# Kernel tuning notes

Measured on AMD Instinct MI355X. Metric: run time of the kernel, lower is better.

## Reference

```python
import jax, jax.numpy as jnp
import numpy as np

STRIDES = (8, 16, 32)
BINS = 16
NC = 80
ALPHA, GAMMA = 0.25, 2.0
W_CLS, W_IOU, W_DFL = 1.0, 7.5, 1.5
B, MAX_GT = 32, 32
EPS = 1e-7


def setup_inputs() -> dict:
    key = jax.random.key(0)
    k0, k1, k2, k3, k4, k5, k6 = jax.random.split(key, 7)
    p0 = jax.random.normal(k0, (B, 4 * BINS + NC, 80, 80), dtype=jnp.float32)
    p1 = jax.random.normal(k1, (B, 4 * BINS + NC, 40, 40), dtype=jnp.float32)
    p2 = jax.random.normal(k2, (B, 4 * BINS + NC, 20, 20), dtype=jnp.float32)
    # realistic xyxy boxes inside a 640x640 image
    c = jax.random.uniform(k3, (B, MAX_GT, 2), minval=60.0, maxval=580.0)
    wh = jax.random.uniform(k4, (B, MAX_GT, 2), minval=16.0, maxval=120.0)
    gt_bboxes = jnp.concatenate([c - wh / 2, c + wh / 2], axis=-1).astype(jnp.float32)
    gt_labels = jax.random.randint(k5, (B, MAX_GT), 0, NC, dtype=jnp.int32)
    raw = jax.random.randint(k6, (B, 8400), 0, 20 * MAX_GT, dtype=jnp.int32)
    matched_gt_inds = jnp.where(raw < MAX_GT, raw, -1)
    return {"p0": p0, "p1": p1, "p2": p2, "gt_bboxes": gt_bboxes,
            "gt_labels": gt_labels, "matched_gt_inds": matched_gt_inds}


def _decode_scale(p, stride):
    # p: [B, 4*BINS + NC, H, W]
    Bp, C, H, W = p.shape
    dfl = p[:, :4 * BINS].reshape(Bp, 4, BINS, H, W)
    cls = p[:, 4 * BINS:]
    # DFL decode: expectation of softmax over bins, scaled by stride
    prob = jax.nn.softmax(dfl, axis=2)
    proj = jnp.arange(BINS, dtype=p.dtype)
    dist = jnp.einsum('bkchw,c->bkhw', prob, proj) * stride  # [B,4,H,W] in pixels
    ys, xs = jnp.meshgrid(jnp.arange(H), jnp.arange(W), indexing='ij')
    cx = ((xs.astype(p.dtype)) + 0.5) * stride
    cy = ((ys.astype(p.dtype)) + 0.5) * stride
    boxes = jnp.stack([cx - dist[:, 0], cy - dist[:, 1],
                       cx + dist[:, 2], cy + dist[:, 3]], axis=-1).reshape(Bp, H * W, 4)
    cls_logits = cls.transpose(0, 2, 3, 1).reshape(Bp, H * W, NC)
    dfl_flat = dfl.transpose(0, 3, 4, 1, 2).reshape(Bp, H * W, 4, BINS)
    grid = jnp.stack([cx, cy], axis=-1).reshape(H * W, 2)
    smap = jnp.full((H * W,), stride, dtype=p.dtype)
    return cls_logits, dfl_flat, boxes, grid, smap


def reference(p0, p1, p2, gt_bboxes, gt_labels, matched_gt_inds):
    outs = [_decode_scale(p, s) for p, s in zip((p0, p1, p2), STRIDES)]
    scores = jnp.concatenate([o[0] for o in outs], axis=1)   # [B,N,NC]
    dfl = jnp.concatenate([o[1] for o in outs], axis=1)      # [B,N,4,BINS]
    pboxes = jnp.concatenate([o[2] for o in outs], axis=1)   # [B,N,4]
    grid = jnp.concatenate([o[3] for o in outs], axis=0)     # [N,2]
    smap = jnp.concatenate([o[4] for o in outs], axis=0)     # [N]

    pos = matched_gt_inds >= 0                               # [B,N]
    idx = jnp.where(pos, matched_gt_inds, 0)
    lbl = jnp.take_along_axis(gt_labels, idx, axis=1)        # [B,N]
    posf = pos.astype(scores.dtype)
    tgt_scores = jax.nn.one_hot(lbl, NC, dtype=scores.dtype) * posf[..., None]

    # sigmoid focal loss (stable BCE-with-logits)
    prob = jax.nn.sigmoid(scores)
    ce = jnp.maximum(scores, 0) - scores * tgt_scores + jnp.log1p(jnp.exp(-jnp.abs(scores)))
    p_t = prob * tgt_scores + (1 - prob) * (1 - tgt_scores)
    alpha_t = tgt_scores * ALPHA + (1 - tgt_scores) * (1 - ALPHA)
    cls_elem = alpha_t * (1.0 - p_t) ** GAMMA * ce
    num_pos = jnp.maximum(posf.sum(), 1.0)
    loss_cls = cls_elem.sum() / num_pos

    # gather matched GT boxes per anchor
    tboxes = jnp.take_along_axis(gt_bboxes, idx[..., None], axis=1)  # [B,N,4]
    gx, gy = grid[None, :, 0], grid[None, :, 1]
    l = jnp.clip(gx - tboxes[..., 0], 0.0)
    t = jnp.clip(gy - tboxes[..., 1], 0.0)
    r = jnp.clip(tboxes[..., 2] - gx, 0.0)
    b_ = jnp.clip(tboxes[..., 3] - gy, 0.0)
    dists = jnp.stack([l, t, r, b_], axis=-1) / smap[None, :, None]   # [B,N,4]
    tb = jnp.clip(dists, 0.0, BINS - 1 - 1e-6)
    lo = jnp.floor(tb).astype(jnp.int32)
    hi = jnp.minimum(lo + 1, BINS - 1)
    a = tb - lo.astype(tb.dtype)
    # soft two-bin DFL target (vectorized form of the scatter_add loop)
    tdist = (jax.nn.one_hot(lo, BINS, dtype=dfl.dtype) * (1.0 - a)[..., None]
             + jax.nn.one_hot(hi, BINS, dtype=dfl.dtype) * a[..., None])   # [B,N,4,BINS]
    logp = jax.nn.log_softmax(dfl, axis=-1)
    dfl_elem = -(tdist * logp).sum(-1)                                # [B,N,4]
    loss_dfl = (dfl_elem * posf[..., None]).sum() / (num_pos * 4.0)

    # IoU loss on positives
    ix1 = jnp.maximum(pboxes[..., 0], tboxes[..., 0])
    iy1 = jnp.maximum(pboxes[..., 1], tboxes[..., 1])
    ix2 = jnp.minimum(pboxes[..., 2], tboxes[..., 2])
    iy2 = jnp.minimum(pboxes[..., 3], tboxes[..., 3])
    inter = jnp.clip(ix2 - ix1, 0.0) * jnp.clip(iy2 - iy1, 0.0)
    area_p = jnp.clip(pboxes[..., 2] - pboxes[..., 0], 0.0) * jnp.clip(pboxes[..., 3] - pboxes[..., 1], 0.0)
    area_t = jnp.clip(tboxes[..., 2] - tboxes[..., 0], 0.0) * jnp.clip(tboxes[..., 3] - tboxes[..., 1], 0.0)
    iou = inter / (area_p + area_t - inter + EPS)
    loss_iou = ((1.0 - iou) * posf).sum() / num_pos

    total = W_CLS * loss_cls + W_IOU * loss_iou + W_DFL * loss_dfl
    return total
```

## Files before the change

kernel.cpp:

```cpp
#include <hip/hip_runtime.h>
#include <math.h>

#define NCLS 80
#define BINS 16
#define BATCH 32
#define MAX_GT 32
#define NA 8400
#define AN (BATCH * NA)
#define NT 2100
#define NQG (BATCH * NT)
#define NB_DFL 263
#define NB_CLS 5120
#define NSLOT 64
#define ALPHA_C 0.25f
#define W_CLS 1.0
#define W_IOU 7.5
#define W_DFL 1.5
#define EPS_F 1e-7f


__device__ __forceinline__ void block_reduce_atomic_16(float val, double* __restrict__ target)
{
    __shared__ float s[16];
    __syncthreads();
    #pragma unroll
    for (int o = 32; o > 0; o >>= 1) val += __shfl_down(val, o);
    const int wave = threadIdx.x >> 6, lane = threadIdx.x & 63;
    if (lane == 0) s[wave] = val;
    __syncthreads();
    if (threadIdx.x == 0) {
        float t = 0.f;
        #pragma unroll
        for (int i = 0; i < 16; ++i) t += s[i];
        atomicAdd(target, (double)t);
    }
}

__device__ __forceinline__ void block_reduce_atomic_4(float val, double* __restrict__ target)
{
    __shared__ float s[4];
    __syncthreads();
    #pragma unroll
    for (int o = 32; o > 0; o >>= 1) val += __shfl_down(val, o);
    const int wave = threadIdx.x >> 6, lane = threadIdx.x & 63;
    if (lane == 0) s[wave] = val;
    __syncthreads();
    if (threadIdx.x == 0) atomicAdd(target, (double)(s[0] + s[1] + s[2] + s[3]));
}

__device__ __forceinline__ float focal_elem(float s, float tt)
{
    float e   = __expf(-fabsf(s));
    float inv = 1.f / (1.f + e);
    float prob = (s >= 0.f) ? inv : e * inv;
    float ce  = fmaxf(s, 0.f) - s * tt + __logf(1.f + e);
    float p_t = prob * tt + (1.f - prob) * (1.f - tt);
    float alpha_t = tt * ALPHA_C + (1.f - tt) * (1.f - ALPHA_C);
    float om = 1.f - p_t;
    return alpha_t * om * om * ce;
}

__device__ __forceinline__ void quad_map(int t, int& HW, int& off, int& gbase,
                                         int& h, int& w0, float& stride)
{
    if (t < 1600)      { HW = 6400; off = t * 4;          gbase = 0;    stride = 8.f;
                         h = t / 20;  w0 = (t - h * 20) * 4; }
    else if (t < 2000) { HW = 1600; off = (t - 1600) * 4; gbase = 6400; stride = 16.f;
                         int u = t - 1600; h = u / 10; w0 = (u - h * 10) * 4; }
    else               { HW = 400;  off = (t - 2000) * 4; gbase = 8000; stride = 32.f;
                         int u = t - 2000; h = u / 5;  w0 = (u - h * 5) * 4; }
}

__global__ __launch_bounds__(256) void yolo_prep(
    const int* __restrict__ matched, const int* __restrict__ gt_labels,
    signed char* __restrict__ lblmap, double* __restrict__ acc)
{
    if (blockIdx.x == 0) acc[threadIdx.x] = 0.0;
    const int qid = blockIdx.x * 256 + threadIdx.x;
    if (qid >= AN / 4) return;
    const int a0 = qid * 4;
    const int b  = a0 / NA;
    const int4 m4 = *(const int4*)(matched + a0);
    const int mm[4] = {m4.x, m4.y, m4.z, m4.w};
    char4 o;
    o.x = (mm[0] >= 0) ? (signed char)gt_labels[b * MAX_GT + mm[0]] : (signed char)-1;
    o.y = (mm[1] >= 0) ? (signed char)gt_labels[b * MAX_GT + mm[1]] : (signed char)-1;
    o.z = (mm[2] >= 0) ? (signed char)gt_labels[b * MAX_GT + mm[2]] : (signed char)-1;
    o.w = (mm[3] >= 0) ? (signed char)gt_labels[b * MAX_GT + mm[3]] : (signed char)-1;
    *(char4*)(lblmap + a0) = o;
}

__global__ __launch_bounds__(1024, 8) void yolo_mega(
    const float* __restrict__ p0, const float* __restrict__ p1, const float* __restrict__ p2,
    const float* __restrict__ gt_bboxes, const int* __restrict__ matched,
    const signed char* __restrict__ lblmap, double* __restrict__ acc)
{
    const int bid  = blockIdx.x;
    const int slot = bid & (NSLOT - 1);

    if (bid < NB_DFL) {
        __shared__ float4 spd[4][256];
        const int local = threadIdx.x & 255;
        const int k     = threadIdx.x >> 8;
        const int qg    = bid * 256 + local;
        const bool valid = (qg < NQG);
        const int qv = valid ? qg : 0;
        const int b  = qv / NT;
        const int t  = qv - b * NT;

        int HW, off, gbase, h, w0; float stride;
        quad_map(t, HW, off, gbase, h, w0, stride);
        const float inv_s = 1.f / stride;
        const float cy = ((float)h + 0.5f) * stride;
        const float* p = (t < 1600) ? p0 : (t < 2000) ? p1 : p2;

        const int4 m4 = *(const int4*)(matched + (size_t)b * NA + gbase + off);
        const int mm[4] = {m4.x, m4.y, m4.z, m4.w};
        int lo[4]; float fr[4]; bool pos[4];
        #pragma unroll
        for (int j = 0; j < 4; ++j) {
            pos[j] = (mm[j] >= 0);
            int idx = pos[j] ? mm[j] : 0;
            float4 tb = *(const float4*)(gt_bboxes + ((size_t)b * MAX_GT + idx) * 4);
            float cx = ((float)(w0 + j) + 0.5f) * stride;
            float d = (k == 0) ? (cx - tb.x) : (k == 1) ? (cy - tb.y)
                    : (k == 2) ? (tb.z - cx) : (tb.w - cy);
            float tval = fminf(fmaxf(d, 0.f) * inv_s, (float)(BINS - 1) - 1e-6f);
            lo[j] = (int)floorf(tval);
            fr[j] = tval - (float)lo[j];
        }

        const float* pc = p + (size_t)(b * 144 + k * BINS) * HW + off;
        float mx[4], se[4], we[4], vlo[4], vhi[4];
        #pragma unroll
        for (int j = 0; j < 4; ++j) { mx[j] = -1e30f; se[j] = 0.f; we[j] = 0.f; vlo[j] = 0.f; vhi[j] = 0.f; }

        #pragma unroll 4
        for (int i = 0; i < BINS; ++i) {
            float4 q = {0.f, 0.f, 0.f, 0.f};
            if (valid) q = *(const float4*)(pc + (size_t)i * HW);
            const float vj[4] = {q.x, q.y, q.z, q.w};
            #pragma unroll
            for (int j = 0; j < 4; ++j) {
                float v = vj[j];
                float nm = fmaxf(mx[j], v);
                float scale = __expf(mx[j] - nm);
                float e = __expf(v - nm);
                se[j] = se[j] * scale + e;
                we[j] = we[j] * scale + (float)i * e;
                mx[j] = nm;
                vlo[j] = (i == lo[j])     ? v : vlo[j];
                vhi[j] = (i == lo[j] + 1) ? v : vhi[j];
            }
        }

        float part = 0.f;
        float pd[4];
        #pragma unroll
        for (int j = 0; j < 4; ++j) {
            pd[j] = (we[j] / se[j]) * stride;
            if (valid && pos[j]) {
                float lse = mx[j] + __logf(se[j]);
                part += -((1.f - fr[j]) * (vlo[j] - lse) + fr[j] * (vhi[j] - lse));
            }
        }
        spd[k][local] = make_float4(pd[0], pd[1], pd[2], pd[3]);
        __syncthreads();

        float iou_part = 0.f, cnt = 0.f;
        if (k == 0 && valid) {
            const float4 q0 = spd[0][local], q1 = spd[1][local];
            const float4 q2 = spd[2][local], q3 = spd[3][local];
            const float l_[4] = {q0.x, q0.y, q0.z, q0.w};
            const float t_[4] = {q1.x, q1.y, q1.z, q1.w};
            const float r_[4] = {q2.x, q2.y, q2.z, q2.w};
            const float b_[4] = {q3.x, q3.y, q3.z, q3.w};
            #pragma unroll
            for (int j = 0; j < 4; ++j) {
                if (pos[j]) {
                    float4 tb = *(const float4*)(gt_bboxes + ((size_t)b * MAX_GT + mm[j]) * 4);
                    float cx = ((float)(w0 + j) + 0.5f) * stride;
                    float px1 = cx - l_[j], py1 = cy - t_[j];
                    float px2 = cx + r_[j], py2 = cy + b_[j];
                    float ix1 = fmaxf(px1, tb.x), iy1 = fmaxf(py1, tb.y);
                    float ix2 = fminf(px2, tb.z), iy2 = fminf(py2, tb.w);
                    float inter  = fmaxf(ix2 - ix1, 0.f) * fmaxf(iy2 - iy1, 0.f);
                    float area_p = fmaxf(px2 - px1, 0.f) * fmaxf(py2 - py1, 0.f);
                    float area_t = fmaxf(tb.z - tb.x, 0.f) * fmaxf(tb.w - tb.y, 0.f);
                    float iou = inter / (area_p + area_t - inter + EPS_F);
                    iou_part += 1.f - iou;
                    cnt += 1.f;
                }
            }
        }
        block_reduce_atomic_16(part,     &acc[2 * NSLOT + slot]);
        block_reduce_atomic_16(iou_part, &acc[1 * NSLOT + slot]);
        block_reduce_atomic_16(cnt,      &acc[3 * NSLOT + slot]);
    } else {
        const int cbid  = bid - NB_DFL;
        const int half  = cbid & 1;
        const int plane = cbid >> 1;
        const int b = plane / NCLS;
        const int c = plane - b * NCLS;
        const size_t cls_ch = (size_t)(b * 144 + 4 * BINS + c);
        const signed char* lb0 = lblmap + b * NA;

        float part = 0.f;
        for (int q = (int)threadIdx.x; q < 1050; q += 1024) {
            const int t = half * 1050 + q;
            const float* p; int HW, off, gbase;
            if (t < 1600)      { p = p0; HW = 6400; off = t * 4;          gbase = 0;    }
            else if (t < 2000) { p = p1; HW = 1600; off = (t - 1600) * 4; gbase = 6400; }
            else               { p = p2; HW = 400;  off = (t - 2000) * 4; gbase = 8000; }

            float4 s4 = *(const float4*)(p + cls_ch * HW + off);
            char4  l4 = *(const char4*)(lb0 + gbase + off);
            part += focal_elem(s4.x, (c == l4.x) ? 1.f : 0.f);
            part += focal_elem(s4.y, (c == l4.y) ? 1.f : 0.f);
            part += focal_elem(s4.z, (c == l4.z) ? 1.f : 0.f);
            part += focal_elem(s4.w, (c == l4.w) ? 1.f : 0.f);
        }
        block_reduce_atomic_16(part, &acc[0 * NSLOT + slot]);
    }
}

__global__ __launch_bounds__(256) void yolo_loss_fused(
    const float* __restrict__ p0, const float* __restrict__ p1, const float* __restrict__ p2,
    const float* __restrict__ gt_bboxes, const int* __restrict__ gt_labels,
    const int* __restrict__ matched, double* __restrict__ acc)
{
    const int a = blockIdx.x * blockDim.x + threadIdx.x;
    const int b = blockIdx.y;
    const int slot = blockIdx.x & (NSLOT - 1);
    float cls_acc = 0.f, iou_acc = 0.f, dfl_acc = 0.f, pos_cnt = 0.f;
    if (a < NA) {
        const float* p; int HW, W; float stride; int off;
        if (a < 6400)      { p = p0; HW = 6400; W = 80; stride = 8.f;  off = a; }
        else if (a < 8000) { p = p1; HW = 1600; W = 40; stride = 16.f; off = a - 6400; }
        else               { p = p2; HW = 400;  W = 20; stride = 32.f; off = a - 8000; }
        const int h = off / W, w = off - h * W;
        const float cx = ((float)w + 0.5f) * stride, cy = ((float)h + 0.5f) * stride;
        const float* pb = p + ((size_t)b * 144) * (size_t)HW + (size_t)off;
        const int m = matched[(size_t)b * NA + a];
        const bool pos = (m >= 0);
        const int idx = pos ? m : 0;
        const int lbl = gt_labels[b * MAX_GT + idx];
        const float* tbp = gt_bboxes + ((size_t)b * MAX_GT + idx) * 4;
        const float tx1 = tbp[0], ty1 = tbp[1], tx2 = tbp[2], ty2 = tbp[3];
        float tdist[4] = {fmaxf(cx - tx1, 0.f) / stride, fmaxf(cy - ty1, 0.f) / stride,
                          fmaxf(tx2 - cx, 0.f) / stride, fmaxf(ty2 - cy, 0.f) / stride};
        float pdv[4]; float dfl_sum = 0.f;
        #pragma unroll
        for (int k = 0; k < 4; ++k) {
            float tv = fminf(tdist[k], (float)(BINS - 1) - 1e-6f);
            int lo = (int)floorf(tv);
            float fr = tv - (float)lo;
            const float* pc = pb + (size_t)(k * BINS) * HW;
            float v[BINS];
            #pragma unroll
            for (int i = 0; i < BINS; ++i) v[i] = pc[(size_t)i * HW];
            float mx = v[0];
            #pragma unroll
            for (int i = 1; i < BINS; ++i) mx = fmaxf(mx, v[i]);
            float se = 0.f, we = 0.f, vlo = 0.f, vhi = 0.f;
            #pragma unroll
            for (int i = 0; i < BINS; ++i) {
                float e = __expf(v[i] - mx);
                se += e; we += (float)i * e;
                vlo = (i == lo) ? v[i] : vlo;
                vhi = (i == lo + 1) ? v[i] : vhi;
            }
            pdv[k] = (we / se) * stride;
            if (pos) { float lse = mx + __logf(se); dfl_sum += -((1.f - fr) * (vlo - lse) + fr * (vhi - lse)); }
        }
        const float* pcls = pb + (size_t)(4 * BINS) * HW;
        #pragma unroll 4
        for (int c = 0; c < NCLS; ++c)
            cls_acc += focal_elem(pcls[(size_t)c * HW], (pos && c == lbl) ? 1.f : 0.f);
        if (pos) {
            float px1 = cx - pdv[0], py1 = cy - pdv[1], px2 = cx + pdv[2], py2 = cy + pdv[3];
            float ix1 = fmaxf(px1, tx1), iy1 = fmaxf(py1, ty1);
            float ix2 = fminf(px2, tx2), iy2 = fminf(py2, ty2);
            float inter  = fmaxf(ix2 - ix1, 0.f) * fmaxf(iy2 - iy1, 0.f);
            float area_p = fmaxf(px2 - px1, 0.f) * fmaxf(py2 - py1, 0.f);
            float area_t = fmaxf(tx2 - tx1, 0.f) * fmaxf(ty2 - ty1, 0.f);
            float iou = inter / (area_p + area_t - inter + EPS_F);
            iou_acc = 1.f - iou; dfl_acc = dfl_sum; pos_cnt = 1.f;
        }
    }
    block_reduce_atomic_4(cls_acc, &acc[0 * NSLOT + slot]);
    block_reduce_atomic_4(iou_acc, &acc[1 * NSLOT + slot]);
    block_reduce_atomic_4(dfl_acc, &acc[2 * NSLOT + slot]);
    block_reduce_atomic_4(pos_cnt, &acc[3 * NSLOT + slot]);
}

__global__ void yolo_loss_finalize(const double* __restrict__ acc, float* __restrict__ out)
{
    double s[4] = {0.0, 0.0, 0.0, 0.0};
    for (int q = 0; q < 4; ++q)
        for (int i = 0; i < NSLOT; ++i) s[q] += acc[q * NSLOT + i];
    double np = s[3] < 1.0 ? 1.0 : s[3];
    double total = W_CLS * s[0] / np + W_IOU * s[1] / np + W_DFL * s[2] / (np * 4.0);
    out[0] = (float)total;
}

extern "C" void kernel_launch(void* const* d_in, const int* in_sizes, int n_in,
                              void* d_out, int out_size, void* d_ws, size_t ws_size,
                              hipStream_t stream)
{
    const float* p0        = (const float*)d_in[0];
    const float* p1        = (const float*)d_in[1];
    const float* p2        = (const float*)d_in[2];
    const float* gt_bboxes = (const float*)d_in[3];
    const int*   gt_labels = (const int*)d_in[4];
    const int*   matched   = (const int*)d_in[5];
    float*  out = (float*)d_out;

    const size_t accBytes = 4 * NSLOT * sizeof(double);
    double*      acc    = (double*)d_ws;
    signed char* lblmap = (signed char*)((char*)d_ws + accBytes);
    const size_t need = accBytes + (size_t)AN;

    if (ws_size >= need) {
        yolo_prep<<<(AN / 4 + 255) / 256, 256, 0, stream>>>(matched, gt_labels, lblmap, acc);
        yolo_mega<<<NB_DFL + NB_CLS, 1024, 0, stream>>>(p0, p1, p2, gt_bboxes, matched,
                                                        lblmap, acc);
    } else {
        (void)hipMemsetAsync(acc, 0, accBytes, stream);
        dim3 g((NA + 255) / 256, BATCH);
        yolo_loss_fused<<<g, 256, 0, stream>>>(p0, p1, p2, gt_bboxes, gt_labels, matched, acc);
    }
    yolo_loss_finalize<<<1, 1, 0, stream>>>(acc, out);
}
```

Before: 228.2 us.

## Map one anchor per thread in DFL blocks with two-pass softmax

```diff
diff --git a/kernel.cpp b/kernel.cpp
--- a/kernel.cpp
+++ b/kernel.cpp
@@ -8,8 +8,7 @@
 #define NA 8400
 #define AN (BATCH * NA)
 #define NT 2100
-#define NQG (BATCH * NT)
-#define NB_DFL 263
+#define NB_DFL 1050
 #define NB_CLS 5120
 #define NSLOT 64
 #define ALPHA_C 0.25f
@@ -58,17 +57,6 @@
     float alpha_t = tt * ALPHA_C + (1.f - tt) * (1.f - ALPHA_C);
     float om = 1.f - p_t;
     return alpha_t * om * om * ce;
-}
-
-__device__ __forceinline__ void quad_map(int t, int& HW, int& off, int& gbase,
-                                         int& h, int& w0, float& stride)
-{
-    if (t < 1600)      { HW = 6400; off = t * 4;          gbase = 0;    stride = 8.f;
-                         h = t / 20;  w0 = (t - h * 20) * 4; }
-    else if (t < 2000) { HW = 1600; off = (t - 1600) * 4; gbase = 6400; stride = 16.f;
-                         int u = t - 1600; h = u / 10; w0 = (u - h * 10) * 4; }
-    else               { HW = 400;  off = (t - 2000) * 4; gbase = 8000; stride = 32.f;
-                         int u = t - 2000; h = u / 5;  w0 = (u - h * 5) * 4; }
 }
 
 __global__ __launch_bounds__(256) void yolo_prep(
@@ -90,7 +78,7 @@
     *(char4*)(lblmap + a0) = o;
 }
 
-__global__ __launch_bounds__(1024, 8) void yolo_mega(
+__global__ __launch_bounds__(1024, 4) void yolo_mega(
     const float* __restrict__ p0, const float* __restrict__ p1, const float* __restrict__ p2,
     const float* __restrict__ gt_bboxes, const int* __restrict__ matched,
     const signed char* __restrict__ lblmap, double* __restrict__ acc)
@@ -99,99 +87,72 @@
     const int slot = bid & (NSLOT - 1);
 
     if (bid < NB_DFL) {
-        __shared__ float4 spd[4][256];
-        const int local = threadIdx.x & 255;
-        const int k     = threadIdx.x >> 8;
-        const int qg    = bid * 256 + local;
-        const bool valid = (qg < NQG);
-        const int qv = valid ? qg : 0;
-        const int b  = qv / NT;
-        const int t  = qv - b * NT;
-
-        int HW, off, gbase, h, w0; float stride;
-        quad_map(t, HW, off, gbase, h, w0, stride);
-        const float inv_s = 1.f / stride;
+        __shared__ float spd[4][1024];
+        const int la = threadIdx.x & 255;
+        const int k  = threadIdx.x >> 8;
+        const int ga = bid * 256 + la;
+        const int b  = ga / NA;
+        const int ai = ga - b * NA;
+
+        const float* p; int HW, off; float stride; int h, w;
+        if (ai < 6400)      { p = p0; HW = 6400; off = ai;        stride = 8.f;
+                              h = off / 80; w = off - h * 80; }
+        else if (ai < 8000) { p = p1; HW = 1600; off = ai - 6400; stride = 16.f;
+                              h = off / 40; w = off - h * 40; }
+        else                { p = p2; HW = 400;  off = ai - 8000; stride = 32.f;
+                              h = off / 20; w = off - h * 20; }
+        const float cx = ((float)w + 0.5f) * stride;
         const float cy = ((float)h + 0.5f) * stride;
-        const float* p = (t < 1600) ? p0 : (t < 2000) ? p1 : p2;
-
-        const int4 m4 = *(const int4*)(matched + (size_t)b * NA + gbase + off);
-        const int mm[4] = {m4.x, m4.y, m4.z, m4.w};
-        int lo[4]; float fr[4]; bool pos[4];
-        #pragma unroll
-        for (int j = 0; j < 4; ++j) {
-            pos[j] = (mm[j] >= 0);
-            int idx = pos[j] ? mm[j] : 0;
-            float4 tb = *(const float4*)(gt_bboxes + ((size_t)b * MAX_GT + idx) * 4);
-            float cx = ((float)(w0 + j) + 0.5f) * stride;
-            float d = (k == 0) ? (cx - tb.x) : (k == 1) ? (cy - tb.y)
-                    : (k == 2) ? (tb.z - cx) : (tb.w - cy);
-            float tval = fminf(fmaxf(d, 0.f) * inv_s, (float)(BINS - 1) - 1e-6f);
-            lo[j] = (int)floorf(tval);
-            fr[j] = tval - (float)lo[j];
-        }
+
+        const int m = matched[(size_t)b * NA + ai];
+        const bool pos = (m >= 0);
+        const int idx = pos ? m : 0;
+        const float4 tb = *(const float4*)(gt_bboxes + ((size_t)b * MAX_GT + idx) * 4);
+
+        float d = (k == 0) ? (cx - tb.x) : (k == 1) ? (cy - tb.y)
+                : (k == 2) ? (tb.z - cx) : (tb.w - cy);
+        float tval = fminf(fmaxf(d, 0.f) / stride, (float)(BINS - 1) - 1e-6f);
+        const int   lo = (int)floorf(tval);
+        const float fr = tval - (float)lo;
 
         const float* pc = p + (size_t)(b * 144 + k * BINS) * HW + off;
-        float mx[4], se[4], we[4], vlo[4], vhi[4];
-        #pragma unroll
-        for (int j = 0; j < 4; ++j) { mx[j] = -1e30f; se[j] = 0.f; we[j] = 0.f; vlo[j] = 0.f; vhi[j] = 0.f; }
-
-        #pragma unroll 4
+        float v[BINS];
+        #pragma unroll
+        for (int i = 0; i < BINS; ++i) v[i] = pc[(size_t)i * HW];
+
+        float mx = v[0];
+        #pragma unroll
+        for (int i = 1; i < BINS; ++i) mx = fmaxf(mx, v[i]);
+        float se = 0.f, we = 0.f, vlo = 0.f, vhi = 0.f;
+        #pragma unroll
         for (int i = 0; i < BINS; ++i) {
-            float4 q = {0.f, 0.f, 0.f, 0.f};
-            if (valid) q = *(const float4*)(pc + (size_t)i * HW);
-            const float vj[4] = {q.x, q.y, q.z, q.w};
-            #pragma unroll
-            for (int j = 0; j < 4; ++j) {
-                float v = vj[j];
-                float nm = fmaxf(mx[j], v);
-                float scale = __expf(mx[j] - nm);
-                float e = __expf(v - nm);
-                se[j] = se[j] * scale + e;
-                we[j] = we[j] * scale + (float)i * e;
-                mx[j] = nm;
-                vlo[j] = (i == lo[j])     ? v : vlo[j];
-                vhi[j] = (i == lo[j] + 1) ? v : vhi[j];
-            }
+            float e = __expf(v[i] - mx);
+            se += e;
+            we += (float)i * e;
+            vlo = (i == lo)     ? v[i] : vlo;
+            vhi = (i == lo + 1) ? v[i] : vhi;
         }
 
         float part = 0.f;
-        float pd[4];
-        #pragma unroll
-        for (int j = 0; j < 4; ++j) {
-            pd[j] = (we[j] / se[j]) * stride;
-            if (valid && pos[j]) {
-                float lse = mx[j] + __logf(se[j]);
-                part += -((1.f - fr[j]) * (vlo[j] - lse) + fr[j] * (vhi[j] - lse));
-            }
-        }
-        spd[k][local] = make_float4(pd[0], pd[1], pd[2], pd[3]);
+        if (pos) {
+            float lse = mx + __logf(se);
+            part = -((1.f - fr) * (vlo - lse) + fr * (vhi - lse));
+        }
+        spd[k][la] = (we / se) * stride;
         __syncthreads();
 
         float iou_part = 0.f, cnt = 0.f;
-        if (k == 0 && valid) {
-            const float4 q0 = spd[0][local], q1 = spd[1][local];
-            const float4 q2 = spd[2][local], q3 = spd[3][local];
-            const float l_[4] = {q0.x, q0.y, q0.z, q0.w};
-            const float t_[4] = {q1.x, q1.y, q1.z, q1.w};
-            const float r_[4] = {q2.x, q2.y, q2.z, q2.w};
-            const float b_[4] = {q3.x, q3.y, q3.z, q3.w};
-            #pragma unroll
-            for (int j = 0; j < 4; ++j) {
-                if (pos[j]) {
-                    float4 tb = *(const float4*)(gt_bboxes + ((size_t)b * MAX_GT + mm[j]) * 4);
-                    float cx = ((float)(w0 + j) + 0.5f) * stride;
-                    float px1 = cx - l_[j], py1 = cy - t_[j];
-                    float px2 = cx + r_[j], py2 = cy + b_[j];
-                    float ix1 = fmaxf(px1, tb.x), iy1 = fmaxf(py1, tb.y);
-                    float ix2 = fminf(px2, tb.z), iy2 = fminf(py2, tb.w);
-                    float inter  = fmaxf(ix2 - ix1, 0.f) * fmaxf(iy2 - iy1, 0.f);
-                    float area_p = fmaxf(px2 - px1, 0.f) * fmaxf(py2 - py1, 0.f);
-                    float area_t = fmaxf(tb.z - tb.x, 0.f) * fmaxf(tb.w - tb.y, 0.f);
-                    float iou = inter / (area_p + area_t - inter + EPS_F);
-                    iou_part += 1.f - iou;
-                    cnt += 1.f;
-                }
-            }
+        if (k == 0 && pos) {
+            float px1 = cx - spd[0][la], py1 = cy - spd[1][la];
+            float px2 = cx + spd[2][la], py2 = cy + spd[3][la];
+            float ix1 = fmaxf(px1, tb.x), iy1 = fmaxf(py1, tb.y);
+            float ix2 = fminf(px2, tb.z), iy2 = fminf(py2, tb.w);
+            float inter  = fmaxf(ix2 - ix1, 0.f) * fmaxf(iy2 - iy1, 0.f);
+            float area_p = fmaxf(px2 - px1, 0.f) * fmaxf(py2 - py1, 0.f);
+            float area_t = fmaxf(tb.z - tb.x, 0.f) * fmaxf(tb.w - tb.y, 0.f);
+            float iou = inter / (area_p + area_t - inter + EPS_F);
+            iou_part = 1.f - iou;
+            cnt = 1.f;
         }
         block_reduce_atomic_16(part,     &acc[2 * NSLOT + slot]);
         block_reduce_atomic_16(iou_part, &acc[1 * NSLOT + slot]);
```

Result: faster. 217.6 us (-4.7%).
